# Kernel optimization log

Measured on AMD Instinct MI355X. Metric: run time of the kernel, lower is better.

## Reference

```python
import jax, jax.numpy as jnp
import numpy as np

N, D, K = 100000, 512, 32
H1, H2 = 512, 256
LN2PI_2 = float(np.log(2.0 * np.pi) / 2.0)


def _glorot(key, shape):
    fan_in, fan_out = shape[0], shape[1]
    limit = np.sqrt(6.0 / (fan_in + fan_out))
    return jax.random.uniform(key, shape, jnp.float32, -limit, limit)


def setup_inputs() -> dict:
    key = jax.random.key(0)
    k0, k1, k2, k3 = jax.random.split(key, 4)
    return {
        "x": jax.random.normal(k0, (N, D), jnp.float32),
        "W1": _glorot(k1, (D, H1)),
        "b1": jnp.zeros((H1,), jnp.float32),
        "W2": _glorot(k2, (H1, H2)),
        "b2": jnp.zeros((H2,), jnp.float32),
        "W3": _glorot(k3, (H2, K)),
        "b3": jnp.zeros((K,), jnp.float32),
    }


def reference(x, W1, b1, W2, b2, W3, b3):
    # instance attention MLP: softplus hiddens, softmax output -> [N, K]
    h = jax.nn.softplus(x @ W1 + b1)
    h = jax.nn.softplus(h @ W2 + b2)
    att = jax.nn.softmax(h @ W3 + b3, axis=-1)

    att_sum = jnp.sum(att, axis=0)  # [K]
    # weighted mean: sum_n x[n,d] * att[n,k] / sum_n att[n,k]  -> [K, D]
    means = (att.T @ x) / att_sum[:, None]
    # weighted variance: E_w[x^2] - mean^2 (algebraic expansion of
    # sum_n (x - mean)^2 * att / sum att, avoids [N,K,D] intermediate)
    ex2 = (att.T @ (x * x)) / att_sum[:, None]  # [K, D]
    vars_ = ex2 - means * means

    # GMM diagonal log-likelihood, expanded to GEMM form:
    inv_v = 1.0 / vars_  # [K, D]
    maha = (x * x) @ inv_v.T - 2.0 * (x @ (means * inv_v).T) \
           + jnp.sum(means * means * inv_v, axis=-1)[None, :]  # [N, K]
    gmm_log = -0.5 * maha - 0.5 * jnp.sum(jnp.log(vars_), axis=-1)[None, :] - D * LN2PI_2
    return gmm_log, vars_
```

## Files before the change

### kernel.cpp

```cpp
#include <hip/hip_runtime.h>
#include <hip/hip_bf16.h>
#include <math.h>

#define NROWS 100000
#define DDIM  512
#define KCL   32
#define H1DIM 512
#define H2DIM 256
#define LN2PI_2 0.9189385332046727f
#define NCHUNK 196
#define NPAD  100352
#define NBLK  784

typedef __attribute__((ext_vector_type(8))) short short8;
typedef __attribute__((ext_vector_type(4))) short shortx4;
typedef __attribute__((ext_vector_type(4))) float floatx4;

__device__ __forceinline__ float softplus_f(float v) {
    return fmaxf(v, 0.f) + __logf(1.f + __expf(-fabsf(v)));
}

__device__ __forceinline__ unsigned short f2bf_rne(float f) {
    unsigned int u = __float_as_uint(f);
    return (unsigned short)((u + 0x7fffu + ((u >> 16) & 1u)) >> 16);
}

__device__ __forceinline__ float bf2f(short v) {
    return __uint_as_float(((unsigned int)(unsigned short)v) << 16);
}

__global__ __launch_bounds__(256) void cvt_x_bf16(
    const float* __restrict__ x, short* __restrict__ xb)
{
    size_t i = ((size_t)blockIdx.x * 256 + threadIdx.x) * 8;
    float4 f0 = *(const float4*)&x[i];
    float4 f1 = *(const float4*)&x[i + 4];
    short8 o;
    o[0] = (short)f2bf_rne(f0.x); o[1] = (short)f2bf_rne(f0.y);
    o[2] = (short)f2bf_rne(f0.z); o[3] = (short)f2bf_rne(f0.w);
    o[4] = (short)f2bf_rne(f1.x); o[5] = (short)f2bf_rne(f1.y);
    o[6] = (short)f2bf_rne(f1.z); o[7] = (short)f2bf_rne(f1.w);
    *(short8*)&xb[i] = o;
}

__global__ __launch_bounds__(256) void cvt_weights(
    const float* __restrict__ W1, const float* __restrict__ W2,
    const float* __restrict__ W3, short* __restrict__ W1T,
    short* __restrict__ W2T, short* __restrict__ W3T)
{
    int idx = blockIdx.x * 256 + threadIdx.x;
    const int n1 = DDIM * H1DIM;
    const int n2 = H1DIM * H2DIM;
    const int n3 = H2DIM * KCL;
    if (idx < n1) {
        int n = idx % H1DIM, k = idx / H1DIM;
        W1T[(size_t)n * DDIM + k] = (short)f2bf_rne(W1[idx]);
    } else if (idx < n1 + n2) {
        int rel = idx - n1;
        int n = rel % H2DIM, k = rel / H2DIM;
        W2T[(size_t)n * H1DIM + k] = (short)f2bf_rne(W2[rel]);
    } else if (idx < n1 + n2 + n3) {
        int rel = idx - n1 - n2;
        int n = rel % KCL, k = rel / KCL;
        W3T[(size_t)n * H2DIM + k] = (short)f2bf_rne(W3[rel]);
    }
}

#define LDP 40
__global__ __launch_bounds__(256) void gemm_sp(
    const short* __restrict__ A, const short* __restrict__ BT,
    const float* __restrict__ bias, void* __restrict__ Cptr,
    int M, int Nc, int Kd, int out_bf16)
{
    __shared__ short As[2][128 * LDP];
    __shared__ short Bs[2][128 * LDP];

    const int tid = threadIdx.x;
    const int lid = tid & 63;
    const int w = tid >> 6;
    const int lm = lid & 15;
    const int lq = lid >> 4;
    const int wrow = (w & 1) * 64;
    const int wcol = (w >> 1) * 64;

    const int nwg = gridDim.x * gridDim.y;
    const int bid = blockIdx.y * gridDim.x + blockIdx.x;
    const int q = nwg >> 3, r = nwg & 7;
    const int xcd = bid & 7, slot = bid >> 3;
    const int L = (xcd < r ? xcd * (q + 1) : r * (q + 1) + (xcd - r) * q) + slot;
    const int row0 = (L / gridDim.x) * 128;
    const int col0 = (L % gridDim.x) * 128;

    const int sr = tid >> 2;
    const int sc = (tid & 3) << 3;

    int gr0 = row0 + sr;       if (gr0 >= M) gr0 = M - 1;
    int gr1 = row0 + 64 + sr;  if (gr1 >= M) gr1 = M - 1;
    const short* Ar0 = A + (size_t)gr0 * Kd + sc;
    const short* Ar1 = A + (size_t)gr1 * Kd + sc;
    const short* Br0 = BT + (size_t)(col0 + sr) * Kd + sc;
    const short* Br1 = BT + (size_t)(col0 + 64 + sr) * Kd + sc;

    floatx4 acc[4][4];
    #pragma unroll
    for (int i = 0; i < 4; i++)
        #pragma unroll
        for (int j = 0; j < 4; j++)
            acc[i][j] = (floatx4){0.f, 0.f, 0.f, 0.f};

    short8 pa0, pa1, pb0, pb1;
    pa0 = *(const short8*)Ar0;
    pa1 = *(const short8*)Ar1;
    pb0 = *(const short8*)Br0;
    pb1 = *(const short8*)Br1;

    const int nk = Kd >> 5;
    for (int kt = 0; kt < nk; kt++) {
        const int buf = kt & 1;
        *(short8*)&As[buf][sr * LDP + sc]        = pa0;
        *(short8*)&As[buf][(64 + sr) * LDP + sc] = pa1;
        *(short8*)&Bs[buf][sr * LDP + sc]        = pb0;
        *(short8*)&Bs[buf][(64 + sr) * LDP + sc] = pb1;
        if (kt + 1 < nk) {
            int ko = (kt + 1) << 5;
            pa0 = *(const short8*)(Ar0 + ko);
            pa1 = *(const short8*)(Ar1 + ko);
            pb0 = *(const short8*)(Br0 + ko);
            pb1 = *(const short8*)(Br1 + ko);
        }
        __syncthreads();

        short8 a[4], b[4];
        #pragma unroll
        for (int i = 0; i < 4; i++)
            a[i] = *(const short8*)&As[buf][(wrow + i * 16 + lm) * LDP + lq * 8];
        #pragma unroll
        for (int j = 0; j < 4; j++)
            b[j] = *(const short8*)&Bs[buf][(wcol + j * 16 + lm) * LDP + lq * 8];
        #pragma unroll
        for (int i = 0; i < 4; i++)
            #pragma unroll
            for (int j = 0; j < 4; j++)
                acc[i][j] = __builtin_amdgcn_mfma_f32_16x16x32_bf16(
                    a[i], b[j], acc[i][j], 0, 0, 0);
    }

    float bb[4];
    #pragma unroll
    for (int j = 0; j < 4; j++)
        bb[j] = bias[col0 + wcol + j * 16 + lm];

    #pragma unroll
    for (int i = 0; i < 4; i++) {
        #pragma unroll
        for (int reg = 0; reg < 4; reg++) {
            int rr = row0 + wrow + i * 16 + lq * 4 + reg;
            if (rr < M) {
                #pragma unroll
                for (int j = 0; j < 4; j++) {
                    int c = col0 + wcol + j * 16 + lm;
                    float v = softplus_f(acc[i][j][reg] + bb[j]);
                    if (out_bf16)
                        ((short*)Cptr)[(size_t)rr * Nc + c] = (short)f2bf_rne(v);
                    else
                        ((float*)Cptr)[(size_t)rr * Nc + c] = v;
                }
            }
        }
    }
}

__global__ __launch_bounds__(256) void logits_mfma(
    const short* __restrict__ h2b, const short* __restrict__ W3T,
    const float* __restrict__ b3, short* __restrict__ attT,
    float* __restrict__ Patt)
{
    __shared__ short Ts[32][136];
    __shared__ float red[4][32];

    const int tid = threadIdx.x;
    const int lane = tid & 63;
    const int lm = lane & 15;
    const int lq = lane >> 4;
    const int w = tid >> 6;
    const int wrow = w * 32;
    const int row0 = blockIdx.x * 128;

    short8 bf[2][8];
    #pragma unroll
    for (int j = 0; j < 2; j++)
        #pragma unroll
        for (int s = 0; s < 8; s++)
            bf[j][s] = *(const short8*)&W3T[(j * 16 + lm) * H2DIM + s * 32 + lq * 8];

    int gr0 = row0 + wrow + lm;      if (gr0 >= NROWS) gr0 = NROWS - 1;
    int gr1 = row0 + wrow + 16 + lm; if (gr1 >= NROWS) gr1 = NROWS - 1;
    const short* a0p = h2b + (size_t)gr0 * H2DIM + lq * 8;
    const short* a1p = h2b + (size_t)gr1 * H2DIM + lq * 8;

    floatx4 acc[2][2];
    #pragma unroll
    for (int i = 0; i < 2; i++)
        #pragma unroll
        for (int j = 0; j < 2; j++)
            acc[i][j] = (floatx4){0.f, 0.f, 0.f, 0.f};

    #pragma unroll
    for (int s = 0; s < 8; s++) {
        short8 a0 = *(const short8*)(a0p + s * 32);
        short8 a1 = *(const short8*)(a1p + s * 32);
        acc[0][0] = __builtin_amdgcn_mfma_f32_16x16x32_bf16(a0, bf[0][s], acc[0][0], 0, 0, 0);
        acc[0][1] = __builtin_amdgcn_mfma_f32_16x16x32_bf16(a0, bf[1][s], acc[0][1], 0, 0, 0);
        acc[1][0] = __builtin_amdgcn_mfma_f32_16x16x32_bf16(a1, bf[0][s], acc[1][0], 0, 0, 0);
        acc[1][1] = __builtin_amdgcn_mfma_f32_16x16x32_bf16(a1, bf[1][s], acc[1][1], 0, 0, 0);
    }

    const float b3v0 = b3[lm];
    const float b3v1 = b3[16 + lm];

    float p0 = 0.f, p1 = 0.f;

    #pragma unroll
    for (int i = 0; i < 2; i++) {
        #pragma unroll
        for (int reg = 0; reg < 4; reg++) {
            const int rloc = wrow + i * 16 + lq * 4 + reg;
            const int rg = row0 + rloc;
            float v0 = acc[i][0][reg] + b3v0;
            float v1 = acc[i][1][reg] + b3v1;
            float m = fmaxf(v0, v1);
            m = fmaxf(m, __shfl_xor(m, 1));
            m = fmaxf(m, __shfl_xor(m, 2));
            m = fmaxf(m, __shfl_xor(m, 4));
            m = fmaxf(m, __shfl_xor(m, 8));
            float e0 = __expf(v0 - m);
            float e1 = __expf(v1 - m);
            float sm = e0 + e1;
            sm += __shfl_xor(sm, 1);
            sm += __shfl_xor(sm, 2);
            sm += __shfl_xor(sm, 4);
            sm += __shfl_xor(sm, 8);
            float inv = 1.f / sm;
            e0 *= inv; e1 *= inv;
            if (rg >= NROWS) { e0 = 0.f; e1 = 0.f; }
            p0 += e0; p1 += e1;
            Ts[lm][rloc]      = (short)f2bf_rne(e0);
            Ts[16 + lm][rloc] = (short)f2bf_rne(e1);
        }
    }

    p0 += __shfl_xor(p0, 16); p0 += __shfl_xor(p0, 32);
    p1 += __shfl_xor(p1, 16); p1 += __shfl_xor(p1, 32);
    if (lq == 0) { red[w][lm] = p0; red[w][16 + lm] = p1; }

    __syncthreads();

    if (tid < KCL)
        Patt[blockIdx.x * KCL + tid] =
            red[0][tid] + red[1][tid] + red[2][tid] + red[3][tid];

    #pragma unroll
    for (int p = 0; p < 2; p++) {
        int u = p * 256 + tid;
        int rr = u >> 4;
        int cs = (u & 15) << 3;
        short8 o = *(const short8*)&Ts[rr][cs];
        *(short8*)&attT[(size_t)rr * NPAD + row0 + cs] = o;
    }
}

__global__ __launch_bounds__(256, 4) void stats_mfma(
    const float* __restrict__ x, const short* __restrict__ attT,
    float* __restrict__ P)
{
    __shared__ short xT[32 * 512];

    const int tid = threadIdx.x;
    const int lane = tid & 63;
    const int lm = lane & 15;
    const int lq = lane >> 4;
    const int w = tid >> 6;
    const int kh = w >> 1;
    const int dh = w & 1;

    const int cblk = blockIdx.x;
    const int dgrp = blockIdx.y;
    const int n0 = cblk * 512;

    short8 afrag[16];
    const short* arow = attT + (size_t)(kh * 16 + lm) * NPAD + n0 + lq * 8;
    #pragma unroll
    for (int s = 0; s < 16; s++)
        afrag[s] = *(const short8*)(arow + s * 32);

    const int c = tid & 31;
    const int rq = tid >> 5;
    const bool full = (n0 + 512 <= NROWS);

    for (int dt = 0; dt < 4; dt++) {
        const int colf = dgrp * 128 + dt * 32 + c;
        __syncthreads();
        if (full) {
            const float* xp = x + (size_t)n0 * DDIM + colf;
            #pragma unroll 4
            for (int p = 0; p < 16; p++) {
                int rr = p * 32 + rq * 4;
                float f0 = xp[(size_t)(rr + 0) * DDIM];
                float f1 = xp[(size_t)(rr + 1) * DDIM];
                float f2 = xp[(size_t)(rr + 2) * DDIM];
                float f3 = xp[(size_t)(rr + 3) * DDIM];
                unsigned int u01 = (unsigned int)f2bf_rne(f0) |
                                   ((unsigned int)f2bf_rne(f1) << 16);
                unsigned int u23 = (unsigned int)f2bf_rne(f2) |
                                   ((unsigned int)f2bf_rne(f3) << 16);
                int boff = (c << 10) + ((rr * 2) ^ ((c & 15) << 4));
                *(uint2*)((char*)xT + boff) = make_uint2(u01, u23);
            }
        } else {
            #pragma unroll 4
            for (int p = 0; p < 16; p++) {
                int rr = p * 32 + rq * 4;
                int g0 = min(n0 + rr + 0, NROWS - 1);
                int g1 = min(n0 + rr + 1, NROWS - 1);
                int g2 = min(n0 + rr + 2, NROWS - 1);
                int g3 = min(n0 + rr + 3, NROWS - 1);
                float f0 = x[(size_t)g0 * DDIM + colf];
                float f1 = x[(size_t)g1 * DDIM + colf];
                float f2 = x[(size_t)g2 * DDIM + colf];
                float f3 = x[(size_t)g3 * DDIM + colf];
                unsigned int u01 = (unsigned int)f2bf_rne(f0) |
                                   ((unsigned int)f2bf_rne(f1) << 16);
                unsigned int u23 = (unsigned int)f2bf_rne(f2) |
                                   ((unsigned int)f2bf_rne(f3) << 16);
                int boff = (c << 10) + ((rr * 2) ^ ((c & 15) << 4));
                *(uint2*)((char*)xT + boff) = make_uint2(u01, u23);
            }
        }
        __syncthreads();

        floatx4 acc1 = (floatx4){0.f, 0.f, 0.f, 0.f};
        floatx4 acc2 = (floatx4){0.f, 0.f, 0.f, 0.f};
        const int rowb = (dh * 16 + lm) << 10;
        #pragma unroll
        for (int s = 0; s < 16; s++) {
            int boff = rowb + ((s * 64 + lq * 16) ^ (lm << 4));
            short8 bx = *(const short8*)((const char*)xT + boff);
            union { short8 s8; unsigned int u[4]; } bq;
            #pragma unroll
            for (int e = 0; e < 4; e++) {
                float f0 = bf2f(bx[2 * e]);
                float f1 = bf2f(bx[2 * e + 1]);
                f0 *= f0; f1 *= f1;
                bq.u[e] = (unsigned int)f2bf_rne(f0) |
                          ((unsigned int)f2bf_rne(f1) << 16);
            }
            acc1 = __builtin_amdgcn_mfma_f32_16x16x32_bf16(
                afrag[s], bx, acc1, 0, 0, 0);
            acc2 = __builtin_amdgcn_mfma_f32_16x16x32_bf16(
                afrag[s], bq.s8, acc2, 0, 0, 0);
        }

        const size_t pbase = (size_t)cblk * 32768 +
                             (size_t)(kh * 16 + lq * 4) * 512 +
                             (size_t)(dgrp * 128 + dt * 32 + dh * 16 + lm);
        #pragma unroll
        for (int reg = 0; reg < 4; reg++) {
            P[pbase + (size_t)reg * 512]         = acc1[reg];
            P[pbase + 16384 + (size_t)reg * 512] = acc2[reg];
        }
    }
}

__global__ __launch_bounds__(256) void stats_reduce(
    const float* __restrict__ P, const float* __restrict__ Patt,
    float* __restrict__ S12, float* __restrict__ att_sum)
{
    int e = blockIdx.x * 256 + threadIdx.x;
    float sum = 0.f;
    for (int cc = 0; cc < NCHUNK; cc++)
        sum += P[(size_t)cc * 32768 + e];
    S12[e] = sum;

    if (blockIdx.x == 0 && threadIdx.x < KCL) {
        float as = 0.f;
        for (int cc = 0; cc < NBLK; cc++) as += Patt[cc * KCL + threadIdx.x];
        att_sum[threadIdx.x] = as;
    }
}

__global__ __launch_bounds__(256) void finalize_stats(
    const float* __restrict__ S12, const float* __restrict__ att_sum,
    short* __restrict__ Bp, float* __restrict__ konst,
    float* __restrict__ vars_out)
{
    int k = blockIdx.x;
    int tid = threadIdx.x;
    __shared__ float red[256];

    float inv_as = 1.f / att_sum[k];
    float csum = 0.f, lsum = 0.f;
    for (int d = tid; d < DDIM; d += 256) {
        float mean = S12[k * DDIM + d] * inv_as;
        float ex2  = S12[KCL * DDIM + k * DDIM + d] * inv_as;
        float var  = ex2 - mean * mean;
        vars_out[k * DDIM + d] = var;
        float iv = 1.f / var;
        Bp[(size_t)k * 1024 + d]       = (short)f2bf_rne(-0.5f * iv);
        Bp[(size_t)k * 1024 + 512 + d] = (short)f2bf_rne(mean * iv);
        csum += mean * mean * iv;
        lsum += logf(var);
    }
    red[tid] = csum;
    __syncthreads();
    for (int s = 128; s > 0; s >>= 1) {
        if (tid < s) red[tid] += red[tid + s];
        __syncthreads();
    }
    float ctot = red[0];
    __syncthreads();
    red[tid] = lsum;
    __syncthreads();
    for (int s = 128; s > 0; s >>= 1) {
        if (tid < s) red[tid] += red[tid + s];
        __syncthreads();
    }
    if (tid == 0)
        konst[k] = -0.5f * ctot - 0.5f * red[0] - DDIM * LN2PI_2;
}

#define LDG 40
__global__ __launch_bounds__(256) void gmm_out_mfma(
    const float* __restrict__ x, const short* __restrict__ Bp,
    const float* __restrict__ konst, float* __restrict__ out)
{
    __shared__ short As_sq[256 * LDG];
    __shared__ short As_x[256 * LDG];

    const int tid = threadIdx.x;
    const int lane = tid & 63;
    const int lm = lane & 15;
    const int lq = lane >> 4;
    const int wid = tid >> 6;
    const int row0 = blockIdx.x * 256;

    floatx4 acc[4][2];
    #pragma unroll
    for (int i = 0; i < 4; i++)
        #pragma unroll
        for (int j = 0; j < 2; j++)
            acc[i][j] = (floatx4){0.f, 0.f, 0.f, 0.f};

    int rrh[8], segh[8], grh[8];
    bool okh[8];
    #pragma unroll
    for (int h = 0; h < 8; h++) {
        int u = tid + h * 256;
        rrh[h] = u >> 3;
        segh[h] = (u & 7) << 2;
        int gr = row0 + rrh[h];
        okh[h] = (gr < NROWS);
        grh[h] = okh[h] ? gr : 0;
    }

    float4 pf[8];
    #pragma unroll
    for (int h = 0; h < 8; h++) {
        float4 v = make_float4(0.f, 0.f, 0.f, 0.f);
        if (okh[h]) v = *(const float4*)&x[(size_t)grh[h] * DDIM + segh[h]];
        pf[h] = v;
    }

    for (int dt = 0; dt < 16; dt++) {
        __syncthreads();
        #pragma unroll
        for (int h = 0; h < 8; h++) {
            float4 v = pf[h];
            shortx4 sx, sq;
            sx[0] = (short)f2bf_rne(v.x); sq[0] = (short)f2bf_rne(v.x * v.x);
            sx[1] = (short)f2bf_rne(v.y); sq[1] = (short)f2bf_rne(v.y * v.y);
            sx[2] = (short)f2bf_rne(v.z); sq[2] = (short)f2bf_rne(v.z * v.z);
            sx[3] = (short)f2bf_rne(v.w); sq[3] = (short)f2bf_rne(v.w * v.w);
            *(shortx4*)&As_x[rrh[h] * LDG + segh[h]]  = sx;
            *(shortx4*)&As_sq[rrh[h] * LDG + segh[h]] = sq;
        }
        if (dt + 1 < 16) {
            #pragma unroll
            for (int h = 0; h < 8; h++) {
                float4 v = make_float4(0.f, 0.f, 0.f, 0.f);
                if (okh[h])
                    v = *(const float4*)&x[(size_t)grh[h] * DDIM +
                                           (dt + 1) * 32 + segh[h]];
                pf[h] = v;
            }
        }
        __syncthreads();

        short8 a_sq[4], a_x[4], b_sq[2], b_x[2];
        #pragma unroll
        for (int i = 0; i < 4; i++) {
            int off = (wid * 64 + i * 16 + lm) * LDG + lq * 8;
            a_sq[i] = *(const short8*)&As_sq[off];
            a_x[i]  = *(const short8*)&As_x[off];
        }
        #pragma unroll
        for (int j = 0; j < 2; j++) {
            const size_t bo = (size_t)(j * 16 + lm) * 1024 + dt * 32 + lq * 8;
            b_sq[j] = *(const short8*)&Bp[bo];
            b_x[j]  = *(const short8*)&Bp[bo + 512];
        }
        #pragma unroll
        for (int i = 0; i < 4; i++)
            #pragma unroll
            for (int j = 0; j < 2; j++) {
                acc[i][j] = __builtin_amdgcn_mfma_f32_16x16x32_bf16(
                    a_sq[i], b_sq[j], acc[i][j], 0, 0, 0);
                acc[i][j] = __builtin_amdgcn_mfma_f32_16x16x32_bf16(
                    a_x[i], b_x[j], acc[i][j], 0, 0, 0);
            }
    }

    float kst[2];
    kst[0] = konst[lm];
    kst[1] = konst[16 + lm];

    #pragma unroll
    for (int i = 0; i < 4; i++) {
        #pragma unroll
        for (int reg = 0; reg < 4; reg++) {
            int rr = row0 + wid * 64 + i * 16 + lq * 4 + reg;
            if (rr < NROWS) {
                out[(size_t)rr * KCL + lm]      = acc[i][0][reg] + kst[0];
                out[(size_t)rr * KCL + 16 + lm] = acc[i][1][reg] + kst[1];
            }
        }
    }
}

extern "C" void kernel_launch(void* const* d_in, const int* in_sizes, int n_in,
                              void* d_out, int out_size, void* d_ws, size_t ws_size,
                              hipStream_t stream)
{
    const float* x  = (const float*)d_in[0];
    const float* W1 = (const float*)d_in[1];
    const float* b1 = (const float*)d_in[2];
    const float* W2 = (const float*)d_in[3];
    const float* b2 = (const float*)d_in[4];
    const float* W3 = (const float*)d_in[5];
    const float* b3 = (const float*)d_in[6];
    float* out = (float*)d_out;

    short* h1b     = (short*)d_ws;
    float* h2      = (float*)(h1b + (size_t)NROWS * H1DIM);
    float* att     = h2 + (size_t)NROWS * H2DIM;
    float* P       = att + (size_t)NROWS * KCL;
    float* PattOld = P + (size_t)NCHUNK * 32768;
    float* S12     = PattOld + NCHUNK * KCL;
    float* att_sum = S12 + 2 * KCL * DDIM;
    short* Bp      = (short*)(att_sum + KCL);
    float* konst   = (float*)(Bp + KCL * 1024);
    (void)ws_size; (void)in_sizes; (void)n_in; (void)out_size; (void)PattOld;

    short* xb   = (short*)h2;
    short* h2b  = (short*)h2;
    short* W1T = (short*)P;
    short* W2T = W1T + H1DIM * DDIM;
    short* W3T = W2T + H2DIM * H1DIM;
    short* attT = h1b;
    float* PattN = att;

    cvt_x_bf16<<<dim3(NROWS * DDIM / 2048), 256, 0, stream>>>(x, xb);
    cvt_weights<<<dim3(1568), 256, 0, stream>>>(W1, W2, W3, W1T, W2T, W3T);

    int mblocks = (NROWS + 127) / 128;

    gemm_sp<<<dim3(H1DIM / 128, mblocks), 256, 0, stream>>>(
        xb, W1T, b1, (void*)h1b, NROWS, H1DIM, DDIM, 1);
    gemm_sp<<<dim3(H2DIM / 128, mblocks), 256, 0, stream>>>(
        h1b, W2T, b2, (void*)h2b, NROWS, H2DIM, H1DIM, 1);
    logits_mfma<<<dim3(NBLK), 256, 0, stream>>>(h2b, W3T, b3, attT, PattN);
    stats_mfma<<<dim3(NCHUNK, 4), 256, 0, stream>>>(x, attT, P);
    stats_reduce<<<dim3(128), 256, 0, stream>>>(P, PattN, S12, att_sum);
    finalize_stats<<<dim3(KCL), 256, 0, stream>>>(
        S12, att_sum, Bp, konst, out + (size_t)NROWS * KCL);
    gmm_out_mfma<<<dim3((NROWS + 255) / 256), 256, 0, stream>>>(x, Bp, konst, out);
}
```

Before: 652.6 us.

## Fuse second MLP GEMM with logits/softmax and read bf16 x downstream

Merges the second hidden-layer GEMM and the logits/softmax kernel into one kernel. Each block computes a 64-row by 256-column h2 tile, stages it in swizzled LDS and runs the K=32 logits MFMA from there, so h2 is never written to or read back from global memory. The stats and GMM output kernels now read the already converted bf16 copy of x instead of fp32 x, which halves their input traffic and removes the per-element conversions. The trade-offs are twice as many smaller blocks with higher LDS use per block, and x^2 computed from bf16-rounded x, which adds rounding error.

Measured after the change: 611.0 us. -6.4%, faster.

```diff
diff --git a/kernel.cpp b/kernel.cpp
--- a/kernel.cpp
+++ b/kernel.cpp
@@ -10,7 +10,7 @@
 #define LN2PI_2 0.9189385332046727f
 #define NCHUNK 196
 #define NPAD  100352
-#define NBLK  784
+#define NBLK2 1568
 
 typedef __attribute__((ext_vector_type(8))) short short8;
 typedef __attribute__((ext_vector_type(4))) short shortx4;
@@ -69,8 +69,8 @@
 #define LDP 40
 __global__ __launch_bounds__(256) void gemm_sp(
     const short* __restrict__ A, const short* __restrict__ BT,
-    const float* __restrict__ bias, void* __restrict__ Cptr,
-    int M, int Nc, int Kd, int out_bf16)
+    const float* __restrict__ bias, short* __restrict__ Cptr,
+    int M, int Nc, int Kd)
 {
     __shared__ short As[2][128 * LDP];
     __shared__ short Bs[2][128 * LDP];
@@ -83,13 +83,8 @@
     const int wrow = (w & 1) * 64;
     const int wcol = (w >> 1) * 64;
 
-    const int nwg = gridDim.x * gridDim.y;
-    const int bid = blockIdx.y * gridDim.x + blockIdx.x;
-    const int q = nwg >> 3, r = nwg & 7;
-    const int xcd = bid & 7, slot = bid >> 3;
-    const int L = (xcd < r ? xcd * (q + 1) : r * (q + 1) + (xcd - r) * q) + slot;
-    const int row0 = (L / gridDim.x) * 128;
-    const int col0 = (L % gridDim.x) * 128;
+    const int row0 = blockIdx.y * 128;
+    const int col0 = blockIdx.x * 128;
 
     const int sr = tid >> 2;
     const int sc = (tid & 3) << 3;
@@ -160,117 +155,190 @@
                 for (int j = 0; j < 4; j++) {
                     int c = col0 + wcol + j * 16 + lm;
                     float v = softplus_f(acc[i][j][reg] + bb[j]);
-                    if (out_bf16)
-                        ((short*)Cptr)[(size_t)rr * Nc + c] = (short)f2bf_rne(v);
-                    else
-                        ((float*)Cptr)[(size_t)rr * Nc + c] = v;
+                    Cptr[(size_t)rr * Nc + c] = (short)f2bf_rne(v);
                 }
             }
         }
     }
 }
 
-__global__ __launch_bounds__(256) void logits_mfma(
-    const short* __restrict__ h2b, const short* __restrict__ W3T,
+__global__ __launch_bounds__(256) void gemm2_logits(
+    const short* __restrict__ h1, const short* __restrict__ W2T,
+    const float* __restrict__ b2, const short* __restrict__ W3T,
     const float* __restrict__ b3, short* __restrict__ attT,
     float* __restrict__ Patt)
 {
-    __shared__ short Ts[32][136];
+    __shared__ __align__(16) short lds[25600];
     __shared__ float red[4][32];
 
+    short* AsB = lds;
+    short* BsB = lds + 2 * 64 * LDP;
+
     const int tid = threadIdx.x;
-    const int lane = tid & 63;
-    const int lm = lane & 15;
-    const int lq = lane >> 4;
+    const int lid = tid & 63;
     const int w = tid >> 6;
-    const int wrow = w * 32;
-    const int row0 = blockIdx.x * 128;
-
-    short8 bf[2][8];
+    const int lm = lid & 15;
+    const int lq = lid >> 4;
+    const int wcol = w * 64;
+
+    const int row0 = blockIdx.x * 64;
+
+    const int sr = tid >> 2;
+    const int sc = (tid & 3) << 3;
+
+    int gr = row0 + sr; if (gr >= NROWS) gr = NROWS - 1;
+    const short* Ar  = h1  + (size_t)gr * H1DIM + sc;
+    const short* Br0 = W2T + (size_t)sr * H1DIM + sc;
+    const short* Br1 = W2T + (size_t)(64 + sr) * H1DIM + sc;
+    const short* Br2 = W2T + (size_t)(128 + sr) * H1DIM + sc;
+    const short* Br3 = W2T + (size_t)(192 + sr) * H1DIM + sc;
+
+    floatx4 acc[4][4];
+    #pragma unroll
+    for (int i = 0; i < 4; i++)
+        #pragma unroll
+        for (int j = 0; j < 4; j++)
+            acc[i][j] = (floatx4){0.f, 0.f, 0.f, 0.f};
+
+    short8 pa, pb0, pb1, pb2, pb3;
+    pa  = *(const short8*)Ar;
+    pb0 = *(const short8*)Br0;
+    pb1 = *(const short8*)Br1;
+    pb2 = *(const short8*)Br2;
+    pb3 = *(const short8*)Br3;
+
+    const int nk = H1DIM >> 5;
+    for (int kt = 0; kt < nk; kt++) {
+        const int buf = kt & 1;
+        *(short8*)&AsB[buf * (64 * LDP) + sr * LDP + sc]          = pa;
+        *(short8*)&BsB[buf * (256 * LDP) + sr * LDP + sc]         = pb0;
+        *(short8*)&BsB[buf * (256 * LDP) + (64 + sr) * LDP + sc]  = pb1;
+        *(short8*)&BsB[buf * (256 * LDP) + (128 + sr) * LDP + sc] = pb2;
+        *(short8*)&BsB[buf * (256 * LDP) + (192 + sr) * LDP + sc] = pb3;
+        if (kt + 1 < nk) {
+            int ko = (kt + 1) << 5;
+            pa  = *(const short8*)(Ar + ko);
+            pb0 = *(const short8*)(Br0 + ko);
+            pb1 = *(const short8*)(Br1 + ko);
+            pb2 = *(const short8*)(Br2 + ko);
+            pb3 = *(const short8*)(Br3 + ko);
+        }
+        __syncthreads();
+
+        short8 a[4], b[4];
+        #pragma unroll
+        for (int i = 0; i < 4; i++)
+            a[i] = *(const short8*)&AsB[buf * (64 * LDP) + (i * 16 + lm) * LDP + lq * 8];
+        #pragma unroll
+        for (int j = 0; j < 4; j++)
+            b[j] = *(const short8*)&BsB[buf * (256 * LDP) + (wcol + j * 16 + lm) * LDP + lq * 8];
+        #pragma unroll
+        for (int i = 0; i < 4; i++)
+            #pragma unroll
+            for (int j = 0; j < 4; j++)
+                acc[i][j] = __builtin_amdgcn_mfma_f32_16x16x32_bf16(
+                    a[i], b[j], acc[i][j], 0, 0, 0);
+    }
+
+    __syncthreads();
+
+    float bb2[4];
+    #pragma unroll
+    for (int j = 0; j < 4; j++)
+        bb2[j] = b2[wcol + j * 16 + lm];
+    #pragma unroll
+    for (int i = 0; i < 4; i++) {
+        #pragma unroll
+        for (int reg = 0; reg < 4; reg++) {
+            const int r = i * 16 + lq * 4 + reg;
+            const int rx = (r & 7) << 4;
+            #pragma unroll
+            for (int j = 0; j < 4; j++) {
+                const int c = wcol + j * 16 + lm;
+                float v = softplus_f(acc[i][j][reg] + bb2[j]);
+                *(short*)((char*)lds + ((r * 512 + c * 2) ^ rx)) =
+                    (short)f2bf_rne(v);
+            }
+        }
+    }
+    __syncthreads();
+
+    short8 bf3[2][8];
     #pragma unroll
     for (int j = 0; j < 2; j++)
         #pragma unroll
         for (int s = 0; s < 8; s++)
-            bf[j][s] = *(const short8*)&W3T[(j * 16 + lm) * H2DIM + s * 32 + lq * 8];
-
-    int gr0 = row0 + wrow + lm;      if (gr0 >= NROWS) gr0 = NROWS - 1;
-    int gr1 = row0 + wrow + 16 + lm; if (gr1 >= NROWS) gr1 = NROWS - 1;
-    const short* a0p = h2b + (size_t)gr0 * H2DIM + lq * 8;
-    const short* a1p = h2b + (size_t)gr1 * H2DIM + lq * 8;
-
-    floatx4 acc[2][2];
-    #pragma unroll
-    for (int i = 0; i < 2; i++)
-        #pragma unroll
-        for (int j = 0; j < 2; j++)
-            acc[i][j] = (floatx4){0.f, 0.f, 0.f, 0.f};
-
+            bf3[j][s] = *(const short8*)&W3T[(j * 16 + lm) * H2DIM + s * 32 + lq * 8];
+
+    floatx4 lacc[2];
+    lacc[0] = (floatx4){0.f, 0.f, 0.f, 0.f};
+    lacc[1] = (floatx4){0.f, 0.f, 0.f, 0.f};
+    const int lr = w * 16 + lm;
+    const int lrx = (lr & 7) << 4;
     #pragma unroll
     for (int s = 0; s < 8; s++) {
-        short8 a0 = *(const short8*)(a0p + s * 32);
-        short8 a1 = *(const short8*)(a1p + s * 32);
-        acc[0][0] = __builtin_amdgcn_mfma_f32_16x16x32_bf16(a0, bf[0][s], acc[0][0], 0, 0, 0);
-        acc[0][1] = __builtin_amdgcn_mfma_f32_16x16x32_bf16(a0, bf[1][s], acc[0][1], 0, 0, 0);
-        acc[1][0] = __builtin_amdgcn_mfma_f32_16x16x32_bf16(a1, bf[0][s], acc[1][0], 0, 0, 0);
-        acc[1][1] = __builtin_amdgcn_mfma_f32_16x16x32_bf16(a1, bf[1][s], acc[1][1], 0, 0, 0);
+        short8 a0 = *(const short8*)((const char*)lds +
+                        ((lr * 512 + s * 64 + lq * 16) ^ lrx));
+        lacc[0] = __builtin_amdgcn_mfma_f32_16x16x32_bf16(a0, bf3[0][s], lacc[0], 0, 0, 0);
+        lacc[1] = __builtin_amdgcn_mfma_f32_16x16x32_bf16(a0, bf3[1][s], lacc[1], 0, 0, 0);
     }
 
     const float b3v0 = b3[lm];
     const float b3v1 = b3[16 + lm];
-
     float p0 = 0.f, p1 = 0.f;
-
-    #pragma unroll
-    for (int i = 0; i < 2; i++) {
-        #pragma unroll
-        for (int reg = 0; reg < 4; reg++) {
-            const int rloc = wrow + i * 16 + lq * 4 + reg;
-            const int rg = row0 + rloc;
-            float v0 = acc[i][0][reg] + b3v0;
-            float v1 = acc[i][1][reg] + b3v1;
-            float m = fmaxf(v0, v1);
-            m = fmaxf(m, __shfl_xor(m, 1));
-            m = fmaxf(m, __shfl_xor(m, 2));
-            m = fmaxf(m, __shfl_xor(m, 4));
-            m = fmaxf(m, __shfl_xor(m, 8));
-            float e0 = __expf(v0 - m);
-            float e1 = __expf(v1 - m);
-            float sm = e0 + e1;
-            sm += __shfl_xor(sm, 1);
-            sm += __shfl_xor(sm, 2);
-            sm += __shfl_xor(sm, 4);
-            sm += __shfl_xor(sm, 8);
-            float inv = 1.f / sm;
-            e0 *= inv; e1 *= inv;
-            if (rg >= NROWS) { e0 = 0.f; e1 = 0.f; }
-            p0 += e0; p1 += e1;
-            Ts[lm][rloc]      = (short)f2bf_rne(e0);
-            Ts[16 + lm][rloc] = (short)f2bf_rne(e1);
-        }
-    }
-
+    float e0s[4], e1s[4];
+    #pragma unroll
+    for (int reg = 0; reg < 4; reg++) {
+        const int rg = row0 + w * 16 + lq * 4 + reg;
+        float v0 = lacc[0][reg] + b3v0;
+        float v1 = lacc[1][reg] + b3v1;
+        float m = fmaxf(v0, v1);
+        m = fmaxf(m, __shfl_xor(m, 1));
+        m = fmaxf(m, __shfl_xor(m, 2));
+        m = fmaxf(m, __shfl_xor(m, 4));
+        m = fmaxf(m, __shfl_xor(m, 8));
+        float e0 = __expf(v0 - m);
+        float e1 = __expf(v1 - m);
+        float sm = e0 + e1;
+        sm += __shfl_xor(sm, 1);
+        sm += __shfl_xor(sm, 2);
+        sm += __shfl_xor(sm, 4);
+        sm += __shfl_xor(sm, 8);
+        float inv = 1.f / sm;
+        e0 *= inv; e1 *= inv;
+        if (rg >= NROWS) { e0 = 0.f; e1 = 0.f; }
+        p0 += e0; p1 += e1;
+        e0s[reg] = e0; e1s[reg] = e1;
+    }
     p0 += __shfl_xor(p0, 16); p0 += __shfl_xor(p0, 32);
     p1 += __shfl_xor(p1, 16); p1 += __shfl_xor(p1, 32);
     if (lq == 0) { red[w][lm] = p0; red[w][16 + lm] = p1; }
 
     __syncthreads();
 
+    short (*Ts)[72] = (short(*)[72])lds;
+    #pragma unroll
+    for (int reg = 0; reg < 4; reg++) {
+        const int rloc = w * 16 + lq * 4 + reg;
+        Ts[lm][rloc]      = (short)f2bf_rne(e0s[reg]);
+        Ts[16 + lm][rloc] = (short)f2bf_rne(e1s[reg]);
+    }
+    __syncthreads();
+
     if (tid < KCL)
         Patt[blockIdx.x * KCL + tid] =
             red[0][tid] + red[1][tid] + red[2][tid] + red[3][tid];
 
-    #pragma unroll
-    for (int p = 0; p < 2; p++) {
-        int u = p * 256 + tid;
-        int rr = u >> 4;
-        int cs = (u & 15) << 3;
-        short8 o = *(const short8*)&Ts[rr][cs];
-        *(short8*)&attT[(size_t)rr * NPAD + row0 + cs] = o;
+    {
+        int rr = tid >> 3;
+        int cs = (tid & 7) << 3;
+        *(short8*)&attT[(size_t)rr * NPAD + row0 + cs] =
+            *(const short8*)&Ts[rr][cs];
     }
 }
 
 __global__ __launch_bounds__(256, 4) void stats_mfma(
-    const float* __restrict__ x, const short* __restrict__ attT,
+    const short* __restrict__ xb, const short* __restrict__ attT,
     float* __restrict__ P)
 {
     __shared__ short xT[32 * 512];
@@ -301,20 +369,17 @@
         const int colf = dgrp * 128 + dt * 32 + c;
         __syncthreads();
         if (full) {
-            const float* xp = x + (size_t)n0 * DDIM + colf;
+            const short* xp = xb + (size_t)n0 * DDIM + colf;
             #pragma unroll 4
             for (int p = 0; p < 16; p++) {
                 int rr = p * 32 + rq * 4;
-                float f0 = xp[(size_t)(rr + 0) * DDIM];
-                float f1 = xp[(size_t)(rr + 1) * DDIM];
-                float f2 = xp[(size_t)(rr + 2) * DDIM];
-                float f3 = xp[(size_t)(rr + 3) * DDIM];
-                unsigned int u01 = (unsigned int)f2bf_rne(f0) |
-                                   ((unsigned int)f2bf_rne(f1) << 16);
-                unsigned int u23 = (unsigned int)f2bf_rne(f2) |
-                                   ((unsigned int)f2bf_rne(f3) << 16);
+                unsigned int h0 = (unsigned short)xp[(size_t)(rr + 0) * DDIM];
+                unsigned int h1 = (unsigned short)xp[(size_t)(rr + 1) * DDIM];
+                unsigned int h2 = (unsigned short)xp[(size_t)(rr + 2) * DDIM];
+                unsigned int h3 = (unsigned short)xp[(size_t)(rr + 3) * DDIM];
                 int boff = (c << 10) + ((rr * 2) ^ ((c & 15) << 4));
-                *(uint2*)((char*)xT + boff) = make_uint2(u01, u23);
+                *(uint2*)((char*)xT + boff) =
+                    make_uint2(h0 | (h1 << 16), h2 | (h3 << 16));
             }
         } else {
             #pragma unroll 4
@@ -324,16 +389,13 @@
                 int g1 = min(n0 + rr + 1, NROWS - 1);
                 int g2 = min(n0 + rr + 2, NROWS - 1);
                 int g3 = min(n0 + rr + 3, NROWS - 1);
-                float f0 = x[(size_t)g0 * DDIM + colf];
-                float f1 = x[(size_t)g1 * DDIM + colf];
-                float f2 = x[(size_t)g2 * DDIM + colf];
-                float f3 = x[(size_t)g3 * DDIM + colf];
-                unsigned int u01 = (unsigned int)f2bf_rne(f0) |
-                                   ((unsigned int)f2bf_rne(f1) << 16);
-                unsigned int u23 = (unsigned int)f2bf_rne(f2) |
-                                   ((unsigned int)f2bf_rne(f3) << 16);
+                unsigned int h0 = (unsigned short)xb[(size_t)g0 * DDIM + colf];
+                unsigned int h1 = (unsigned short)xb[(size_t)g1 * DDIM + colf];
+                unsigned int h2 = (unsigned short)xb[(size_t)g2 * DDIM + colf];
+                unsigned int h3 = (unsigned short)xb[(size_t)g3 * DDIM + colf];
                 int boff = (c << 10) + ((rr * 2) ^ ((c & 15) << 4));
-                *(uint2*)((char*)xT + boff) = make_uint2(u01, u23);
+                *(uint2*)((char*)xT + boff) =
+                    make_uint2(h0 | (h1 << 16), h2 | (h3 << 16));
             }
         }
         __syncthreads();
@@ -383,7 +445,7 @@
 
     if (blockIdx.x == 0 && threadIdx.x < KCL) {
         float as = 0.f;
-        for (int cc = 0; cc < NBLK; cc++) as += Patt[cc * KCL + threadIdx.x];
+        for (int cc = 0; cc < NBLK2; cc++) as += Patt[cc * KCL + threadIdx.x];
         att_sum[threadIdx.x] = as;
     }
 }
@@ -430,7 +492,7 @@
 
 #define LDG 40
 __global__ __launch_bounds__(256) void gmm_out_mfma(
-    const float* __restrict__ x, const short* __restrict__ Bp,
+    const short* __restrict__ xb, const short* __restrict__ Bp,
     const float* __restrict__ konst, float* __restrict__ out)
 {
     __shared__ short As_sq[256 * LDG];
@@ -462,11 +524,11 @@
         grh[h] = okh[h] ? gr : 0;
     }
 
-    float4 pf[8];
+    shortx4 pf[8];
     #pragma unroll
     for (int h = 0; h < 8; h++) {
-        float4 v = make_float4(0.f, 0.f, 0.f, 0.f);
-        if (okh[h]) v = *(const float4*)&x[(size_t)grh[h] * DDIM + segh[h]];
+        shortx4 v = (shortx4){0, 0, 0, 0};
+        if (okh[h]) v = *(const shortx4*)&xb[(size_t)grh[h] * DDIM + segh[h]];
         pf[h] = v;
     }
 
@@ -474,22 +536,23 @@
         __syncthreads();
         #pragma unroll
         for (int h = 0; h < 8; h++) {
-            float4 v = pf[h];
-            shortx4 sx, sq;
-            sx[0] = (short)f2bf_rne(v.x); sq[0] = (short)f2bf_rne(v.x * v.x);
-            sx[1] = (short)f2bf_rne(v.y); sq[1] = (short)f2bf_rne(v.y * v.y);
-            sx[2] = (short)f2bf_rne(v.z); sq[2] = (short)f2bf_rne(v.z * v.z);
-            sx[3] = (short)f2bf_rne(v.w); sq[3] = (short)f2bf_rne(v.w * v.w);
+            shortx4 sx = pf[h];
+            shortx4 sq;
+            #pragma unroll
+            for (int e = 0; e < 4; e++) {
+                float f = bf2f(sx[e]);
+                sq[e] = (short)f2bf_rne(f * f);
+            }
             *(shortx4*)&As_x[rrh[h] * LDG + segh[h]]  = sx;
             *(shortx4*)&As_sq[rrh[h] * LDG + segh[h]] = sq;
         }
         if (dt + 1 < 16) {
             #pragma unroll
             for (int h = 0; h < 8; h++) {
-                float4 v = make_float4(0.f, 0.f, 0.f, 0.f);
+                shortx4 v = (shortx4){0, 0, 0, 0};
                 if (okh[h])
-                    v = *(const float4*)&x[(size_t)grh[h] * DDIM +
-                                           (dt + 1) * 32 + segh[h]];
+                    v = *(const shortx4*)&xb[(size_t)grh[h] * DDIM +
+                                             (dt + 1) * 32 + segh[h]];
                 pf[h] = v;
             }
         }
@@ -560,13 +623,12 @@
     float* konst   = (float*)(Bp + KCL * 1024);
     (void)ws_size; (void)in_sizes; (void)n_in; (void)out_size; (void)PattOld;
 
-    short* xb   = (short*)h2;
-    short* h2b  = (short*)h2;
+    short* xb = (short*)h2;
+    short* attT  = (short*)att;
+    float* PattN = (float*)(attT + (size_t)KCL * NPAD);
     short* W1T = (short*)P;
     short* W2T = W1T + H1DIM * DDIM;
     short* W3T = W2T + H2DIM * H1DIM;
-    short* attT = h1b;
-    float* PattN = att;
 
     cvt_x_bf16<<<dim3(NROWS * DDIM / 2048), 256, 0, stream>>>(x, xb);
     cvt_weights<<<dim3(1568), 256, 0, stream>>>(W1, W2, W3, W1T, W2T, W3T);
@@ -574,13 +636,13 @@
     int mblocks = (NROWS + 127) / 128;
 
     gemm_sp<<<dim3(H1DIM / 128, mblocks), 256, 0, stream>>>(
-        xb, W1T, b1, (void*)h1b, NROWS, H1DIM, DDIM, 1);
-    gemm_sp<<<dim3(H2DIM / 128, mblocks), 256, 0, stream>>>(
-        h1b, W2T, b2, (void*)h2b, NROWS, H2DIM, H1DIM, 1);
-    logits_mfma<<<dim3(NBLK), 256, 0, stream>>>(h2b, W3T, b3, attT, PattN);
-    stats_mfma<<<dim3(NCHUNK, 4), 256, 0, stream>>>(x, attT, P);
+        xb, W1T, b1, h1b, NROWS, H1DIM, DDIM);
+    gemm2_logits<<<dim3(NBLK2), 256, 0, stream>>>(
+        h1b, W2T, b2, W3T, b3, attT, PattN);
+    stats_mfma<<<dim3(NCHUNK, 4), 256, 0, stream>>>(xb, attT, P);
     stats_reduce<<<dim3(128), 256, 0, stream>>>(P, PattN, S12, att_sum);
     finalize_stats<<<dim3(KCL), 256, 0, stream>>>(
         S12, att_sum, Bp, konst, out + (size_t)NROWS * KCL);
-    gmm_out_mfma<<<dim3((NROWS + 255) / 256), 256, 0, stream>>>(x, Bp, konst, out);
-}
+    gmm_out_mfma<<<dim3((NROWS + 255) / 256), 256, 0, stream>>>(
+        xb, Bp, konst, out);
+}
```
